# Kernel optimization log

Hardware: AMD Instinct MI355X
Metric: run time of the kernel (lower is better)

Reference implementation:

```python
import jax, jax.numpy as jnp
import numpy as np


def _dependence(X):
    # X: [N, D]. dom[i, j] = True iff X[i, d] > X[j, d] for all d.
    # Diagonal is automatically False (X[i] > X[i] is all False), matching the
    # original's explicit i != j exclusion.
    dom = jnp.all(X[:, None, :] > X[None, :, :], axis=-1)  # [N, N] bool
    n = X.shape[0]
    Z = dom.sum(axis=1).astype(X.dtype) / (n - 1)  # [N]
    return Z


def setup_inputs() -> dict:
    key = jax.random.key(0)
    k1, k2 = jax.random.split(key)
    N, D = 8192, 8
    X = jax.random.normal(k1, (N, D), dtype=jnp.float32)
    X_hat = jax.random.normal(k2, (N, D), dtype=jnp.float32)
    return {"X": X, "X_hat": X_hat}


def reference(X, X_hat):
    Z = jnp.sort(_dependence(X))
    Zhat = jnp.sort(_dependence(X_hat))
    return jnp.sum(jnp.abs(Z - Zhat)) / Z.shape[0]
```

## Files before the change

kernel.cpp:

```cpp
#include <hip/hip_runtime.h>

constexpr int N = 8192;
constexpr int BLK = 256;
constexpr int JSPLIT = 32;
constexpr int JSEG = N / JSPLIT;

typedef float f32x4 __attribute__((ext_vector_type(4)));
typedef uint32_t u32x16 __attribute__((ext_vector_type(16)));

#define SLOAD16(dst, base, immstr) \
  asm volatile("s_load_dwordx16 %0, %1, " immstr : "=s"(dst) : "s"(base))

__device__ __forceinline__ float max3f(float a, float b, float c) {
  float r;
  asm("v_max3_f32 %0, %1, %2, %3" : "=v"(r) : "v"(a), "v"(b), "v"(c));
  return r;
}
__device__ __forceinline__ float max2f(float a, float b) {
  float r;
  asm("v_max_f32 %0, %1, %2" : "=v"(r) : "v"(a), "v"(b));
  return r;
}

#define JROW(q, e)                                                       \
  {                                                                      \
    const float d0 = __uint_as_float(q[e + 0]) - xi0;                    \
    const float d1 = __uint_as_float(q[e + 1]) - xi1;                    \
    const float d2 = __uint_as_float(q[e + 2]) - xi2;                    \
    const float d3 = __uint_as_float(q[e + 3]) - xi3;                    \
    const float d4 = __uint_as_float(q[e + 4]) - xi4;                    \
    const float d5 = __uint_as_float(q[e + 5]) - xi5;                    \
    const float d6 = __uint_as_float(q[e + 6]) - xi6;                    \
    const float d7 = __uint_as_float(q[e + 7]) - xi7;                    \
    const float t0 = max3f(d0, d1, d2);                                  \
    const float t1 = max3f(d3, d4, d5);                                  \
    const float t2 = max3f(d6, d7, t0);                                  \
    cnt += (max2f(t1, t2) < 0.0f) ? 1 : 0;                               \
  }

__global__ __launch_bounds__(BLK, 4) void dom_count_kernel(
    const float* __restrict__ X, const float* __restrict__ Xh,
    int* __restrict__ counts) {
  const float* __restrict__ M = (blockIdx.z == 0) ? X : Xh;
  int* cnt_out = counts + blockIdx.z * N;

  const int i = blockIdx.x * BLK + threadIdx.x;

  const f32x4* Mi = reinterpret_cast<const f32x4*>(M + (size_t)i * 8);
  const f32x4 ra = Mi[0];
  const f32x4 rb = Mi[1];
  const float xi0 = ra.x, xi1 = ra.y, xi2 = ra.z, xi3 = ra.w;
  const float xi4 = rb.x, xi5 = rb.y, xi6 = rb.z, xi7 = rb.w;

  int cnt = 0;
  const float* jb = M + (size_t)(blockIdx.y * JSEG) * 8;
  for (int jj = 0; jj < JSEG; jj += 8) {
    u32x16 q0, q1, q2, q3;
    const float* gb = jb + (size_t)jj * 8;
    SLOAD16(q0, gb, "0x0");
    SLOAD16(q1, gb, "0x40");
    SLOAD16(q2, gb, "0x80");
    SLOAD16(q3, gb, "0xC0");
    asm volatile("s_waitcnt lgkmcnt(0)"
                 : "+s"(q0), "+s"(q1), "+s"(q2), "+s"(q3));
    JROW(q0, 0)
    JROW(q0, 8)
    JROW(q1, 0)
    JROW(q1, 8)
    JROW(q2, 0)
    JROW(q2, 8)
    JROW(q3, 0)
    JROW(q3, 8)
  }

  atomicAdd(&cnt_out[i], cnt);
}

constexpr int HB = 16;
__global__ __launch_bounds__(1024) void hist_partial_kernel(
    const int* __restrict__ counts, int* __restrict__ ghist) {
  __shared__ int lhist[N];
  const int tid = threadIdx.x;
  for (int q = tid; q < N; q += 1024) lhist[q] = 0;
  __syncthreads();

  const int k = blockIdx.x * (2 * N / HB) + tid;
  const int v = counts[k];
  atomicAdd(&lhist[v], (k < N) ? 1 : -1);
  __syncthreads();

#pragma unroll
  for (int q = 0; q < N / 1024; ++q) {
    const int bin = tid * (N / 1024) + q;
    const int h = lhist[bin];
    if (h != 0) atomicAdd(&ghist[bin], h);
  }
}

__global__ __launch_bounds__(1024) void finalize_kernel(
    const int* __restrict__ ghist, float* __restrict__ out) {
  __shared__ int wsum[16];
  __shared__ int wexc[16];
  __shared__ int wabs[16];

  const int tid = threadIdx.x;
  const int lane = tid & 63;
  const int wid = tid >> 6;

  int local[8];
  int s = 0;
#pragma unroll
  for (int q = 0; q < 8; ++q) {
    local[q] = ghist[tid * 8 + q];
    s += local[q];
  }

  int incl = s;
#pragma unroll
  for (int off = 1; off < 64; off <<= 1) {
    const int v = __shfl_up(incl, off);
    if (lane >= off) incl += v;
  }
  if (lane == 63) wsum[wid] = incl;
  __syncthreads();

  if (tid == 0) {
    int acc = 0;
#pragma unroll
    for (int w = 0; w < 16; ++w) { wexc[w] = acc; acc += wsum[w]; }
  }
  __syncthreads();

  int run = wexc[wid] + (incl - s);
  int acc = 0;
#pragma unroll
  for (int q = 0; q < 8; ++q) {
    run += local[q];
    acc += (run < 0) ? -run : run;
  }

#pragma unroll
  for (int off = 32; off > 0; off >>= 1) acc += __shfl_down(acc, off);
  if (lane == 0) wabs[wid] = acc;
  __syncthreads();

  if (tid == 0) {
    int total = 0;
#pragma unroll
    for (int w = 0; w < 16; ++w) total += wabs[w];
    out[0] = (float)((double)total / ((double)(N - 1) * (double)N));
  }
}

extern "C" void kernel_launch(void* const* d_in, const int* in_sizes, int n_in,
                              void* d_out, int out_size, void* d_ws, size_t ws_size,
                              hipStream_t stream) {
  const float* X = (const float*)d_in[0];
  const float* Xh = (const float*)d_in[1];
  float* out = (float*)d_out;
  int* counts = (int*)d_ws;
  int* ghist = counts + 2 * N;

  hipMemsetAsync(counts, 0, 3 * N * sizeof(int), stream);

  dim3 grid(N / BLK, JSPLIT, 2);
  dom_count_kernel<<<grid, BLK, 0, stream>>>(X, Xh, counts);
  hist_partial_kernel<<<HB, 1024, 0, stream>>>(counts, ghist);
  finalize_kernel<<<1, 1024, 0, stream>>>(ghist, out);
}
```

Before: 107.2 us.

## Sort rows by first dimension to skip impossible dominance tiles

Rows are ranked by their first coordinate using a brute-force 64-bit key rank pass, then scattered into sorted order. Since row i can only dominate row j if X[i,0] > X[j,0], the dominance kernel only needs tiles where the j chunk is at or below the i chunk, which roughly halves the pairwise work. The inner comparison is also rewritten as hand-scheduled assembly using a carry-add count. The cost is three extra kernels (key, O(N^2/8) rank, scatter) plus a larger workspace, with a fallback flat path when the workspace is too small.

```diff
diff --git a/kernel.cpp b/kernel.cpp
--- a/kernel.cpp
+++ b/kernel.cpp
@@ -1,51 +1,111 @@
 #include <hip/hip_runtime.h>
+#include <stdint.h>
 
 constexpr int N = 8192;
 constexpr int BLK = 256;
-constexpr int JSPLIT = 32;
-constexpr int JSEG = N / JSPLIT;
+constexpr int NCH = N / BLK;
+constexpr int JSPLIT_R = 8;
+constexpr int JSEG_R = N / JSPLIT_R;
 
 typedef float f32x4 __attribute__((ext_vector_type(4)));
 typedef uint32_t u32x16 __attribute__((ext_vector_type(16)));
+typedef uint64_t u64x8 __attribute__((ext_vector_type(8)));
 
 #define SLOAD16(dst, base, immstr) \
   asm volatile("s_load_dwordx16 %0, %1, " immstr : "=s"(dst) : "s"(base))
 
-__device__ __forceinline__ float max3f(float a, float b, float c) {
-  float r;
-  asm("v_max3_f32 %0, %1, %2, %3" : "=v"(r) : "v"(a), "v"(b), "v"(c));
-  return r;
-}
-__device__ __forceinline__ float max2f(float a, float b) {
-  float r;
-  asm("v_max_f32 %0, %1, %2" : "=v"(r) : "v"(a), "v"(b));
-  return r;
-}
-
-#define JROW(q, e)                                                       \
-  {                                                                      \
-    const float d0 = __uint_as_float(q[e + 0]) - xi0;                    \
-    const float d1 = __uint_as_float(q[e + 1]) - xi1;                    \
-    const float d2 = __uint_as_float(q[e + 2]) - xi2;                    \
-    const float d3 = __uint_as_float(q[e + 3]) - xi3;                    \
-    const float d4 = __uint_as_float(q[e + 4]) - xi4;                    \
-    const float d5 = __uint_as_float(q[e + 5]) - xi5;                    \
-    const float d6 = __uint_as_float(q[e + 6]) - xi6;                    \
-    const float d7 = __uint_as_float(q[e + 7]) - xi7;                    \
-    const float t0 = max3f(d0, d1, d2);                                  \
-    const float t1 = max3f(d3, d4, d5);                                  \
-    const float t2 = max3f(d6, d7, t0);                                  \
-    cnt += (max2f(t1, t2) < 0.0f) ? 1 : 0;                               \
-  }
-
-__global__ __launch_bounds__(BLK, 4) void dom_count_kernel(
+#define JROW8(q, e)                                                          \
+  {                                                                          \
+    float t0, t1, t2, t3, t4, t5, t6, t7;                                    \
+    asm volatile(                                                            \
+        "v_sub_f32 %[t0], %[a0], %[x0]\n\t"                                  \
+        "v_sub_f32 %[t1], %[a1], %[x1]\n\t"                                  \
+        "v_sub_f32 %[t2], %[a2], %[x2]\n\t"                                  \
+        "v_sub_f32 %[t3], %[a3], %[x3]\n\t"                                  \
+        "v_sub_f32 %[t4], %[a4], %[x4]\n\t"                                  \
+        "v_sub_f32 %[t5], %[a5], %[x5]\n\t"                                  \
+        "v_sub_f32 %[t6], %[a6], %[x6]\n\t"                                  \
+        "v_sub_f32 %[t7], %[a7], %[x7]\n\t"                                  \
+        "v_max3_f32 %[t0], %[t0], %[t1], %[t2]\n\t"                          \
+        "v_max3_f32 %[t3], %[t3], %[t4], %[t5]\n\t"                          \
+        "v_max3_f32 %[t6], %[t6], %[t7], %[t0]\n\t"                          \
+        "v_max_f32 %[t3], %[t3], %[t6]\n\t"                                  \
+        "v_cmp_gt_f32 vcc, 0, %[t3]\n\t"                                     \
+        "v_addc_co_u32 %[c], vcc, 0, %[c], vcc"                              \
+        : [c] "+v"(cnt), [t0] "=&v"(t0), [t1] "=&v"(t1), [t2] "=&v"(t2),     \
+          [t3] "=&v"(t3), [t4] "=&v"(t4), [t5] "=&v"(t5), [t6] "=&v"(t6),    \
+          [t7] "=&v"(t7)                                                     \
+        : [a0] "s"(q[e + 0]), [a1] "s"(q[e + 1]), [a2] "s"(q[e + 2]),        \
+          [a3] "s"(q[e + 3]), [a4] "s"(q[e + 4]), [a5] "s"(q[e + 5]),        \
+          [a6] "s"(q[e + 6]), [a7] "s"(q[e + 7]), [x0] "v"(xi0),             \
+          [x1] "v"(xi1), [x2] "v"(xi2), [x3] "v"(xi3), [x4] "v"(xi4),        \
+          [x5] "v"(xi5), [x6] "v"(xi6), [x7] "v"(xi7)                        \
+        : "vcc");                                                            \
+  }
+
+#define KEYCMP(kj)                                      \
+  asm volatile(                                         \
+      "v_cmp_lt_u64 vcc, %[a], %[b]\n\t"                \
+      "v_addc_co_u32 %[c], vcc, 0, %[c], vcc"           \
+      : [c] "+v"(cnt)                                   \
+      : [a] "s"(kj), [b] "v"(ki)                        \
+      : "vcc");
+
+__device__ __forceinline__ uint64_t sortkey(float f, int idx) {
+  uint32_t b = __float_as_uint(f);
+  uint32_t m = (uint32_t)((int32_t)b >> 31);
+  uint32_t s = b ^ (m | 0x80000000u);
+  return ((uint64_t)s << 13) | (uint32_t)idx;
+}
+
+
+__global__ __launch_bounds__(BLK) void key_kernel(
     const float* __restrict__ X, const float* __restrict__ Xh,
-    int* __restrict__ counts) {
-  const float* __restrict__ M = (blockIdx.z == 0) ? X : Xh;
-  int* cnt_out = counts + blockIdx.z * N;
-
+    uint64_t* __restrict__ keys) {
+  const int r = blockIdx.x * BLK + threadIdx.x;
+  const int m = r >> 13, i = r & (N - 1);
+  const float d0 = (m ? Xh : X)[(size_t)i * 8];
+  keys[r] = sortkey(d0, i);
+}
+
+__global__ __launch_bounds__(BLK, 8) void rank_kernel(
+    const uint64_t* __restrict__ keys, int* __restrict__ rank) {
+  const int m = blockIdx.z;
+  const uint64_t* __restrict__ K = keys + (size_t)m * N;
   const int i = blockIdx.x * BLK + threadIdx.x;
-
+  const uint64_t ki = K[i];
+  int cnt = 0;
+  const uint64_t* jb = K + (size_t)blockIdx.y * JSEG_R;
+  for (int jj = 0; jj < JSEG_R; jj += 8) {
+    u64x8 q;
+    SLOAD16(q, jb + jj, "0x0");
+    asm volatile("s_waitcnt lgkmcnt(0)" : "+s"(q));
+    KEYCMP(q[0]) KEYCMP(q[1]) KEYCMP(q[2]) KEYCMP(q[3])
+    KEYCMP(q[4]) KEYCMP(q[5]) KEYCMP(q[6]) KEYCMP(q[7])
+  }
+  atomicAdd(&rank[(size_t)m * N + i], cnt);
+}
+
+__global__ __launch_bounds__(BLK) void scatter_kernel(
+    const float* __restrict__ X, const float* __restrict__ Xh,
+    const int* __restrict__ rank, float* __restrict__ Xs) {
+  const int r = blockIdx.x * BLK + threadIdx.x;
+  const int m = r >> 13, i = r & (N - 1);
+  const f32x4* src = reinterpret_cast<const f32x4*>((m ? Xh : X) + (size_t)i * 8);
+  f32x4* dst = reinterpret_cast<f32x4*>(Xs + (size_t)m * N * 8 +
+                                        (size_t)rank[r] * 8);
+  dst[0] = src[0];
+  dst[1] = src[1];
+}
+
+__global__ __launch_bounds__(BLK, 8) void dom_count_kernel(
+    const float* __restrict__ Xs, int* __restrict__ counts) {
+  const int ib = blockIdx.x, jc = blockIdx.y, m = blockIdx.z;
+  if (jc > ib) return;
+  const float* __restrict__ M = Xs + (size_t)m * N * 8;
+  int* cnt_out = counts + (size_t)m * N;
+
+  const int i = ib * BLK + threadIdx.x;
   const f32x4* Mi = reinterpret_cast<const f32x4*>(M + (size_t)i * 8);
   const f32x4 ra = Mi[0];
   const f32x4 rb = Mi[1];
@@ -53,8 +113,8 @@
   const float xi4 = rb.x, xi5 = rb.y, xi6 = rb.z, xi7 = rb.w;
 
   int cnt = 0;
-  const float* jb = M + (size_t)(blockIdx.y * JSEG) * 8;
-  for (int jj = 0; jj < JSEG; jj += 8) {
+  const float* jb = M + (size_t)(jc * BLK) * 8;
+  for (int jj = 0; jj < BLK; jj += 8) {
     u32x16 q0, q1, q2, q3;
     const float* gb = jb + (size_t)jj * 8;
     SLOAD16(q0, gb, "0x0");
@@ -63,16 +123,41 @@
     SLOAD16(q3, gb, "0xC0");
     asm volatile("s_waitcnt lgkmcnt(0)"
                  : "+s"(q0), "+s"(q1), "+s"(q2), "+s"(q3));
-    JROW(q0, 0)
-    JROW(q0, 8)
-    JROW(q1, 0)
-    JROW(q1, 8)
-    JROW(q2, 0)
-    JROW(q2, 8)
-    JROW(q3, 0)
-    JROW(q3, 8)
-  }
-
+    JROW8(q0, 0) JROW8(q0, 8)
+    JROW8(q1, 0) JROW8(q1, 8)
+    JROW8(q2, 0) JROW8(q2, 8)
+    JROW8(q3, 0) JROW8(q3, 8)
+  }
+  atomicAdd(&cnt_out[i], cnt);
+}
+
+__global__ __launch_bounds__(BLK, 8) void dom_flat_kernel(
+    const float* __restrict__ X, const float* __restrict__ Xh,
+    int* __restrict__ counts) {
+  const float* __restrict__ M = (blockIdx.z == 0) ? X : Xh;
+  int* cnt_out = counts + (size_t)blockIdx.z * N;
+  const int i = blockIdx.x * BLK + threadIdx.x;
+  const f32x4* Mi = reinterpret_cast<const f32x4*>(M + (size_t)i * 8);
+  const f32x4 ra = Mi[0];
+  const f32x4 rb = Mi[1];
+  const float xi0 = ra.x, xi1 = ra.y, xi2 = ra.z, xi3 = ra.w;
+  const float xi4 = rb.x, xi5 = rb.y, xi6 = rb.z, xi7 = rb.w;
+  int cnt = 0;
+  const float* jb = M + (size_t)(blockIdx.y * BLK) * 8;
+  for (int jj = 0; jj < BLK; jj += 8) {
+    u32x16 q0, q1, q2, q3;
+    const float* gb = jb + (size_t)jj * 8;
+    SLOAD16(q0, gb, "0x0");
+    SLOAD16(q1, gb, "0x40");
+    SLOAD16(q2, gb, "0x80");
+    SLOAD16(q3, gb, "0xC0");
+    asm volatile("s_waitcnt lgkmcnt(0)"
+                 : "+s"(q0), "+s"(q1), "+s"(q2), "+s"(q3));
+    JROW8(q0, 0) JROW8(q0, 8)
+    JROW8(q1, 0) JROW8(q1, 8)
+    JROW8(q2, 0) JROW8(q2, 8)
+    JROW8(q3, 0) JROW8(q3, 8)
+  }
   atomicAdd(&cnt_out[i], cnt);
 }
 
@@ -158,13 +243,24 @@
   const float* X = (const float*)d_in[0];
   const float* Xh = (const float*)d_in[1];
   float* out = (float*)d_out;
+
   int* counts = (int*)d_ws;
   int* ghist = counts + 2 * N;
-
-  hipMemsetAsync(counts, 0, 3 * N * sizeof(int), stream);
-
-  dim3 grid(N / BLK, JSPLIT, 2);
-  dom_count_kernel<<<grid, BLK, 0, stream>>>(X, Xh, counts);
+  int* rank = counts + 3 * N;
+  uint64_t* keys = (uint64_t*)(counts + 5 * N);
+  float* Xs = (float*)(keys + 2 * N);
+  const size_t needed = (size_t)5 * N * 4 + (size_t)2 * N * 8 + (size_t)16 * N * 4;
+
+  if (ws_size >= needed) {
+    hipMemsetAsync(counts, 0, (size_t)5 * N * sizeof(int), stream);
+    key_kernel<<<2 * N / BLK, BLK, 0, stream>>>(X, Xh, keys);
+    rank_kernel<<<dim3(NCH, JSPLIT_R, 2), BLK, 0, stream>>>(keys, rank);
+    scatter_kernel<<<2 * N / BLK, BLK, 0, stream>>>(X, Xh, rank, Xs);
+    dom_count_kernel<<<dim3(NCH, NCH, 2), BLK, 0, stream>>>(Xs, counts);
+  } else {
+    hipMemsetAsync(counts, 0, (size_t)3 * N * sizeof(int), stream);
+    dom_flat_kernel<<<dim3(NCH, NCH, 2), BLK, 0, stream>>>(X, Xh, counts);
+  }
   hist_partial_kernel<<<HB, 1024, 0, stream>>>(counts, ghist);
   finalize_kernel<<<1, 1024, 0, stream>>>(ghist, out);
 }
```

Result: slower. 154.1 us (+43.7%).
